# Performance work log

Hardware: AMD Instinct MI355X
Metric: run time of the kernel (lower is better)

Reference implementation:

```python
import jax, jax.numpy as jnp
import numpy as np

NEG_SLOPE = 0.2  # PyG GATConv default


def add_self_loops(edge_index, num_nodes):
    loops = jnp.arange(num_nodes, dtype=edge_index.dtype)
    return jnp.concatenate([edge_index, jnp.stack([loops, loops])], axis=1)


def gat_conv(x, edge_index, W, att_src, att_dst, bias, heads, out_ch, concat):
    # x: [N, F_in]; edge_index: [2, E] with row0=src(j), row1=dst(i)
    N = x.shape[0]
    xl = (x @ W).reshape(N, heads, out_ch)              # [N, H, C]
    src, dst = edge_index[0], edge_index[1]
    a_src = jnp.einsum('nhc,hc->nh', xl, att_src)        # [N, H]
    a_dst = jnp.einsum('nhc,hc->nh', xl, att_dst)        # [N, H]
    alpha = jax.nn.leaky_relu(a_src[src] + a_dst[dst], NEG_SLOPE)  # [E, H]
    # segment softmax over incoming edges of each dst node
    m = jax.ops.segment_max(alpha, dst, num_segments=N)  # [N, H]
    e = jnp.exp(alpha - m[dst])
    denom = jax.ops.segment_sum(e, dst, num_segments=N)
    coef = e / (denom[dst] + 1e-16)                      # [E, H]
    msg = xl[src] * coef[..., None]                      # [E, H, C]
    out = jax.ops.segment_sum(msg, dst, num_segments=N)  # [N, H, C]
    out = out.reshape(N, heads * out_ch) if concat else out.mean(axis=1)
    return out + bias


def setup_inputs() -> dict:
    key = jax.random.key(0)
    ks = jax.random.split(key, 12)
    N, E = 50000, 800000
    nfeat, nhid, nheads, nclass = 512, 8, 8, 16
    hid = nhid * nheads  # 64
    s1 = 1.0 / np.sqrt(nfeat)
    s2 = 1.0 / np.sqrt(hid)
    return {
        'x': jax.random.normal(ks[0], (N, nfeat), jnp.float32),
        'edge_index': jax.random.randint(ks[1], (2, E), 0, N, jnp.int64 if jax.config.jax_enable_x64 else jnp.int32),
        'W1': jax.random.uniform(ks[2], (nfeat, hid), jnp.float32, -s1, s1),
        'att_src1': jax.random.uniform(ks[3], (nheads, nhid), jnp.float32, -s2, s2),
        'att_dst1': jax.random.uniform(ks[4], (nheads, nhid), jnp.float32, -s2, s2),
        'bias1': jnp.zeros((hid,), jnp.float32),
        'W2': jax.random.uniform(ks[5], (hid, nclass), jnp.float32, -s2, s2),
        'att_src2': jax.random.uniform(ks[6], (1, nclass), jnp.float32, -0.25, 0.25),
        'att_dst2': jax.random.uniform(ks[7], (1, nclass), jnp.float32, -0.25, 0.25),
        'bias2': jnp.zeros((nclass,), jnp.float32),
    }


def reference(x, edge_index, W1, att_src1, att_dst1, bias1, W2, att_src2, att_dst2, bias2):
    N = x.shape[0]
    ei = add_self_loops(edge_index, N)
    # dropout layers are identity at inference
    h = gat_conv(x, ei, W1, att_src1, att_dst1, bias1, heads=8, out_ch=8, concat=True)
    o = gat_conv(h, ei, W2, att_src2, att_dst2, bias2, heads=1, out_ch=16, concat=True)
    o = jax.nn.elu(o)
    return jax.nn.log_softmax(o, axis=1)
```

## Files before the change

### kernel.cpp

```cpp
#include <hip/hip_runtime.h>
#include <math.h>

#define NEG_SLOPE 0.2f

typedef short short8 __attribute__((ext_vector_type(8)));
typedef float floatx4 __attribute__((ext_vector_type(4)));

static __device__ __forceinline__ float bf2f(unsigned short u) {
  return __uint_as_float(((unsigned int)u) << 16);
}
static __device__ __forceinline__ unsigned short f2bf(float f) {
  unsigned int u = __float_as_uint(f);
  u = (u + 0x7fffu + ((u >> 16) & 1u)) >> 16;
  return (unsigned short)u;
}
static __device__ __forceinline__ unsigned int pack2(float a, float b) {
  return (unsigned int)f2bf(a) | ((unsigned int)f2bf(b) << 16);
}

__global__ void conv_w1(const float* __restrict__ W1, unsigned short* __restrict__ W1t) {
  int i = blockIdx.x * 256 + threadIdx.x;
  int k = i >> 6, c = i & 63;
  W1t[c * 512 + k] = f2bf(W1[i]);
}

__global__ __launch_bounds__(256) void gemm1_mfma(const float* __restrict__ A,
                                                  const unsigned short* __restrict__ W1t,
                                                  const float* __restrict__ att_src,
                                                  const float* __restrict__ att_dst,
                                                  unsigned short* __restrict__ xlb,
                                                  float* __restrict__ a_src,
                                                  float* __restrict__ a_dst, int M) {
  __shared__ unsigned short As[64 * 72];
  __shared__ unsigned short Bs[64 * 72];
  int tid = threadIdx.x;
  int w = tid >> 6, lane = tid & 63;
  int q = lane >> 4, cl = lane & 15;
  int row0 = blockIdx.x << 6;
  floatx4 acc[4] = {};

  int sr = tid >> 2;
  int skq = (tid & 3) << 4;
  int arow = row0 + sr;
  const float* Aptr = A + (size_t)arow * 512 + skq;
  const unsigned short* Bptr = W1t + sr * 512 + skq;
  unsigned short* AsW = As + sr * 72 + skq;
  unsigned short* BsW = Bs + sr * 72 + skq;

  for (int k0 = 0; k0 < 512; k0 += 64) {
    float4 f0 = make_float4(0.f, 0.f, 0.f, 0.f), f1 = f0, f2 = f0, f3 = f0;
    if (arow < M) {
      f0 = *(const float4*)(Aptr + k0);
      f1 = *(const float4*)(Aptr + k0 + 4);
      f2 = *(const float4*)(Aptr + k0 + 8);
      f3 = *(const float4*)(Aptr + k0 + 12);
    }
    uint4 b0 = *(const uint4*)(Bptr + k0);
    uint4 b1 = *(const uint4*)(Bptr + k0 + 8);
    __syncthreads();
    uint4 a0, a1;
    a0.x = pack2(f0.x, f0.y); a0.y = pack2(f0.z, f0.w);
    a0.z = pack2(f1.x, f1.y); a0.w = pack2(f1.z, f1.w);
    a1.x = pack2(f2.x, f2.y); a1.y = pack2(f2.z, f2.w);
    a1.z = pack2(f3.x, f3.y); a1.w = pack2(f3.z, f3.w);
    *(uint4*)(AsW) = a0;
    *(uint4*)(AsW + 8) = a1;
    *(uint4*)(BsW) = b0;
    *(uint4*)(BsW + 8) = b1;
    __syncthreads();
#pragma unroll
    for (int kk = 0; kk < 2; ++kk) {
      short8 af = *(const short8*)(As + (w * 16 + cl) * 72 + kk * 32 + q * 8);
#pragma unroll
      for (int t = 0; t < 4; ++t) {
        short8 bf = *(const short8*)(Bs + (t * 16 + cl) * 72 + kk * 32 + q * 8);
        acc[t] = __builtin_amdgcn_mfma_f32_16x16x32_bf16(af, bf, acc[t], 0, 0, 0);
      }
    }
  }

  float asv[4], adv[4];
#pragma unroll
  for (int t = 0; t < 4; ++t) {
    asv[t] = att_src[t * 16 + cl];
    adv[t] = att_dst[t * 16 + cl];
  }
#pragma unroll
  for (int reg = 0; reg < 4; ++reg) {
    int r = row0 + w * 16 + q * 4 + reg;
    bool ok = r < M;
#pragma unroll
    for (int t = 0; t < 4; ++t) {
      float v = acc[t][reg];
      if (ok) xlb[(size_t)r * 64 + t * 16 + cl] = f2bf(v);
      float ps = v * asv[t];
      float pd = v * adv[t];
      ps += __shfl_xor(ps, 1); pd += __shfl_xor(pd, 1);
      ps += __shfl_xor(ps, 2); pd += __shfl_xor(pd, 2);
      ps += __shfl_xor(ps, 4); pd += __shfl_xor(pd, 4);
      if (ok && (cl & 7) == 0) {
        int h = t * 2 + (cl >> 3);
        a_src[r * 8 + h] = ps;
        a_dst[r * 8 + h] = pd;
      }
    }
  }
}

__global__ void deg_init(int* __restrict__ deg, int N) {
  int n = blockIdx.x * blockDim.x + threadIdx.x;
  if (n < N) deg[n] = 1;
}

__global__ __launch_bounds__(256) void deg_hist_sliced(const int* __restrict__ ei,
                                                       int* __restrict__ deg,
                                                       int E, int N, int ipc) {
  int slice = blockIdx.x & 7;
  int chunk = blockIdx.x >> 3;
  int lo = (int)(((long long)slice * N) >> 3);
  int hi = (int)(((long long)(slice + 1) * N) >> 3);
  int beg = chunk * ipc;
  int end = min(beg + ipc, E);
  for (int i = beg + threadIdx.x; i < end; i += 256) {
    int d = ei[E + i];
    if (d >= lo && d < hi) atomicAdd(&deg[d], 1);
  }
}

__global__ __launch_bounds__(256) void partial_sums(const int* __restrict__ deg,
                                                    int* __restrict__ partials, int N) {
  __shared__ int ws[4];
  int base = blockIdx.x * 512;
  int tid = threadIdx.x;
  int i0 = base + tid * 2;
  int s = 0;
  if (i0 < N) s += deg[i0];
  if (i0 + 1 < N) s += deg[i0 + 1];
#pragma unroll
  for (int off = 32; off >= 1; off >>= 1) s += __shfl_xor(s, off, 64);
  if ((tid & 63) == 0) ws[tid >> 6] = s;
  __syncthreads();
  if (tid == 0) partials[blockIdx.x] = ws[0] + ws[1] + ws[2] + ws[3];
}

__global__ __launch_bounds__(256) void scan_partials(const int* __restrict__ partials,
                                                     int* __restrict__ blockoff,
                                                     int* __restrict__ rowptr, int nb, int N) {
  __shared__ int sums[256];
  int tid = threadIdx.x;
  int chunk = (nb + 255) >> 8;
  int start = tid * chunk, end = min(start + chunk, nb);
  int s = 0;
  for (int i = start; i < end; ++i) s += partials[i];
  sums[tid] = s;
  __syncthreads();
  for (int off = 1; off < 256; off <<= 1) {
    int t = (tid >= off) ? sums[tid - off] : 0;
    __syncthreads();
    sums[tid] += t;
    __syncthreads();
  }
  int run = (tid == 0) ? 0 : sums[tid - 1];
  for (int i = start; i < end; ++i) {
    blockoff[i] = run;
    run += partials[i];
  }
  if (tid == 255) rowptr[N] = sums[255];
}

__global__ __launch_bounds__(256) void scan_blocks(const int* __restrict__ deg,
                                                   const int* __restrict__ blockoff,
                                                   int* __restrict__ rowptr,
                                                   int* __restrict__ cursor, int N) {
  __shared__ int wavesum[4];
  int base = blockIdx.x * 512;
  int tid = threadIdx.x;
  int lane = tid & 63, wv = tid >> 6;
  int i0 = base + tid * 2;
  int d0 = (i0 < N) ? deg[i0] : 0;
  int d1 = (i0 + 1 < N) ? deg[i0 + 1] : 0;
  int s = d0 + d1;
  int v = s;
#pragma unroll
  for (int off = 1; off < 64; off <<= 1) {
    int t = __shfl_up(v, off, 64);
    if (lane >= off) v += t;
  }
  if (lane == 63) wavesum[wv] = v;
  __syncthreads();
  int woff = 0;
  for (int w = 0; w < wv; ++w) woff += wavesum[w];
  int excl = v - s + woff + blockoff[blockIdx.x];
  if (i0 < N) { rowptr[i0] = excl; cursor[i0] = excl; }
  if (i0 + 1 < N) { rowptr[i0 + 1] = excl + d0; cursor[i0 + 1] = excl + d0; }
}

__global__ __launch_bounds__(256) void scatter_sliced(const int* __restrict__ ei,
                                                      int* __restrict__ cursor,
                                                      int* __restrict__ srcs,
                                                      int E, int N, int ipc) {
  int slice = blockIdx.x & 7;
  int chunk = blockIdx.x >> 3;
  int lo = (int)(((long long)slice * N) >> 3);
  int hi = (int)(((long long)(slice + 1) * N) >> 3);
  int total = E + N;
  int beg = chunk * ipc;
  int end = min(beg + ipc, total);
  for (int i = beg + threadIdx.x; i < end; i += 256) {
    int d = (i < E) ? ei[E + i] : (i - E);
    if (d >= lo && d < hi) {
      int s = (i < E) ? ei[i] : d;
      int pos = atomicAdd(&cursor[d], 1);
      srcs[pos] = s;
    }
  }
}

__global__ __launch_bounds__(256) void agg1_csr(const int* __restrict__ rowptr,
                                                const int* __restrict__ srcs,
                                                const float* __restrict__ a_src,
                                                const float* __restrict__ a_dst,
                                                const unsigned short* __restrict__ xlb,
                                                float* __restrict__ agg1, int N) {
  int wave = (blockIdx.x * blockDim.x + threadIdx.x) >> 6;
  int lane = threadIdx.x & 63;
  if (wave >= N) return;
  int h = lane >> 3;
  int beg = rowptr[wave], end = rowptr[wave + 1];
  float ad = a_dst[wave * 8 + h];
  float den = 0.f, acc = 0.f;
  int p = beg;
  for (; p + 4 <= end; p += 4) {
    int s0 = srcs[p], s1 = srcs[p + 1], s2 = srcs[p + 2], s3 = srcs[p + 3];
    float a0 = a_src[s0 * 8 + h], a1 = a_src[s1 * 8 + h];
    float a2 = a_src[s2 * 8 + h], a3 = a_src[s3 * 8 + h];
    float x0 = bf2f(xlb[(size_t)s0 * 64 + lane]);
    float x1 = bf2f(xlb[(size_t)s1 * 64 + lane]);
    float x2 = bf2f(xlb[(size_t)s2 * 64 + lane]);
    float x3 = bf2f(xlb[(size_t)s3 * 64 + lane]);
    a0 += ad; a1 += ad; a2 += ad; a3 += ad;
    a0 = a0 >= 0.f ? a0 : NEG_SLOPE * a0;
    a1 = a1 >= 0.f ? a1 : NEG_SLOPE * a1;
    a2 = a2 >= 0.f ? a2 : NEG_SLOPE * a2;
    a3 = a3 >= 0.f ? a3 : NEG_SLOPE * a3;
    float w0 = __expf(a0), w1 = __expf(a1), w2 = __expf(a2), w3 = __expf(a3);
    den += (w0 + w1) + (w2 + w3);
    acc += w0 * x0 + w1 * x1 + w2 * x2 + w3 * x3;
  }
  for (; p < end; ++p) {
    int s = srcs[p];
    float a = a_src[s * 8 + h] + ad;
    a = a >= 0.f ? a : NEG_SLOPE * a;
    float w = __expf(a);
    den += w;
    acc += w * bf2f(xlb[(size_t)s * 64 + lane]);
  }
  agg1[(size_t)wave * 64 + lane] = acc / (den + 1e-16f);
}

__global__ __launch_bounds__(256) void gemm2_prep(const float* __restrict__ agg1,
                                                  const float* __restrict__ bias1,
                                                  const float* __restrict__ W2,
                                                  const float* __restrict__ att_src2,
                                                  const float* __restrict__ att_dst2,
                                                  float* __restrict__ xl2,
                                                  float* __restrict__ a_src2,
                                                  float* __restrict__ a_dst2, int N) {
  __shared__ float hs[16 * 68];
  int tid = threadIdx.x;
  int n0 = blockIdx.x << 4;
  {
    int node = tid >> 4;
    int off = (tid & 15) << 2;
    int nn = n0 + node;
    float4 v = make_float4(0.f, 0.f, 0.f, 0.f);
    if (nn < N) {
      v = *(const float4*)(agg1 + (size_t)nn * 64 + off);
      float4 b = *(const float4*)(bias1 + off);
      v.x += b.x; v.y += b.y; v.z += b.z; v.w += b.w;
    }
    *(float4*)(hs + node * 68 + off) = v;
  }
  __syncthreads();
  int t = tid >> 4, c = tid & 15;
  int n = n0 + t;
  if (n >= N) return;
  float sum = 0.f;
#pragma unroll
  for (int k = 0; k < 64; ++k) sum += hs[t * 68 + k] * W2[k * 16 + c];
  xl2[(size_t)n * 16 + c] = sum;
  float ps = sum * att_src2[c];
  float pd = sum * att_dst2[c];
#pragma unroll
  for (int w = 8; w >= 1; w >>= 1) {
    ps += __shfl_xor(ps, w, 16);
    pd += __shfl_xor(pd, w, 16);
  }
  if (c == 0) {
    a_src2[n] = ps;
    a_dst2[n] = pd;
  }
}

__global__ __launch_bounds__(256) void agg2_fin(const int* __restrict__ rowptr,
                                                const int* __restrict__ srcs,
                                                const float* __restrict__ a_src2,
                                                const float* __restrict__ a_dst2,
                                                const float* __restrict__ xl2,
                                                const float* __restrict__ bias2,
                                                float* __restrict__ out, int N) {
  int t = blockIdx.x * blockDim.x + threadIdx.x;
  int node = t >> 4;
  int c = t & 15;
  if (node >= N) return;
  int beg = rowptr[node], end = rowptr[node + 1];
  float ad = a_dst2[node];
  float den = 0.f, acc = 0.f;
  int p = beg;
  for (; p + 4 <= end; p += 4) {
    int s0 = srcs[p], s1 = srcs[p + 1], s2 = srcs[p + 2], s3 = srcs[p + 3];
    float a0 = a_src2[s0], a1 = a_src2[s1], a2 = a_src2[s2], a3 = a_src2[s3];
    float x0 = xl2[(size_t)s0 * 16 + c], x1 = xl2[(size_t)s1 * 16 + c];
    float x2 = xl2[(size_t)s2 * 16 + c], x3 = xl2[(size_t)s3 * 16 + c];
    a0 += ad; a1 += ad; a2 += ad; a3 += ad;
    a0 = a0 >= 0.f ? a0 : NEG_SLOPE * a0;
    a1 = a1 >= 0.f ? a1 : NEG_SLOPE * a1;
    a2 = a2 >= 0.f ? a2 : NEG_SLOPE * a2;
    a3 = a3 >= 0.f ? a3 : NEG_SLOPE * a3;
    float w0 = __expf(a0), w1 = __expf(a1), w2 = __expf(a2), w3 = __expf(a3);
    den += (w0 + w1) + (w2 + w3);
    acc += w0 * x0 + w1 * x1 + w2 * x2 + w3 * x3;
  }
  for (; p < end; ++p) {
    int s = srcs[p];
    float a = a_src2[s] + ad;
    a = a >= 0.f ? a : NEG_SLOPE * a;
    float w = __expf(a);
    den += w;
    acc += w * xl2[(size_t)s * 16 + c];
  }
  float o = acc / (den + 1e-16f) + bias2[c];
  o = o > 0.f ? o : expm1f(o);
  float mx = o;
#pragma unroll
  for (int w = 8; w >= 1; w >>= 1) mx = fmaxf(mx, __shfl_xor(mx, w, 16));
  float e = __expf(o - mx);
  float ssum = e;
#pragma unroll
  for (int w = 8; w >= 1; w >>= 1) ssum += __shfl_xor(ssum, w, 16);
  out[(size_t)node * 16 + c] = o - mx - logf(ssum);
}

extern "C" void kernel_launch(void* const* d_in, const int* in_sizes, int n_in,
                              void* d_out, int out_size, void* d_ws, size_t ws_size,
                              hipStream_t stream) {
  const float* x        = (const float*)d_in[0];
  const int*   ei       = (const int*)d_in[1];
  const float* W1       = (const float*)d_in[2];
  const float* att_src1 = (const float*)d_in[3];
  const float* att_dst1 = (const float*)d_in[4];
  const float* bias1    = (const float*)d_in[5];
  const float* W2       = (const float*)d_in[6];
  const float* att_src2 = (const float*)d_in[7];
  const float* att_dst2 = (const float*)d_in[8];
  const float* bias2    = (const float*)d_in[9];
  float* out = (float*)d_out;

  int N = in_sizes[0] / 512;
  int E = in_sizes[1] / 2;
  int nb = (N + 511) / 512;

  char* ws = (char*)d_ws;
  unsigned short* xlb = (unsigned short*)ws;        ws += (size_t)N * 64 * 2;
  unsigned short* W1t = (unsigned short*)ws;        ws += (size_t)512 * 64 * 2;
  float* a_src1 = (float*)ws;                       ws += (size_t)N * 8 * 4;
  float* a_dst1 = (float*)ws;                       ws += (size_t)N * 8 * 4;
  float* agg1   = (float*)ws;                       ws += (size_t)N * 64 * 4;
  float* xl2    = (float*)ws;                       ws += (size_t)N * 16 * 4;
  float* a_src2 = (float*)ws;                       ws += (size_t)N * 4;
  float* a_dst2 = (float*)ws;                       ws += (size_t)N * 4;
  int* deg      = (int*)ws;                         ws += (size_t)N * 4;
  int* rowptr   = (int*)ws;                         ws += (size_t)(N + 1) * 4;
  int* cursor   = (int*)ws;                         ws += (size_t)N * 4;
  int* srcs     = (int*)ws;                         ws += (size_t)(E + N) * 4;
  int* partials = (int*)ws;                         ws += (size_t)nb * 4;
  int* blockoff = (int*)ws;                         ws += (size_t)nb * 4;

  const int NCHUNK = 256;
  int ipc_h = (E + NCHUNK - 1) / NCHUNK;
  int ipc_s = (E + N + NCHUNK - 1) / NCHUNK;
  deg_init<<<(N + 255) / 256, 256, 0, stream>>>(deg, N);
  deg_hist_sliced<<<NCHUNK * 8, 256, 0, stream>>>(ei, deg, E, N, ipc_h);
  partial_sums<<<nb, 256, 0, stream>>>(deg, partials, N);
  scan_partials<<<1, 256, 0, stream>>>(partials, blockoff, rowptr, nb, N);
  scan_blocks<<<nb, 256, 0, stream>>>(deg, blockoff, rowptr, cursor, N);
  scatter_sliced<<<NCHUNK * 8, 256, 0, stream>>>(ei, cursor, srcs, E, N, ipc_s);

  conv_w1<<<128, 256, 0, stream>>>(W1, W1t);
  gemm1_mfma<<<(N + 63) / 64, 256, 0, stream>>>(x, W1t, att_src1, att_dst1,
                                                xlb, a_src1, a_dst1, N);
  agg1_csr<<<((size_t)N * 64 + 255) / 256, 256, 0, stream>>>(rowptr, srcs, a_src1, a_dst1,
                                                             xlb, agg1, N);

  gemm2_prep<<<(N + 15) / 16, 256, 0, stream>>>(agg1, bias1, W2, att_src2, att_dst2,
                                                xl2, a_src2, a_dst2, N);
  agg2_fin<<<((size_t)N * 16 + 255) / 256, 256, 0, stream>>>(rowptr, srcs, a_src2, a_dst2,
                                                             xl2, bias2, out, N);
}
```

Before: 329.6 us.

## Fuse layer-1 aggregation with layer-2 GEMM, double-buffer gemm1, merge prep kernels

The layer-1 CSR aggregation and the layer-2 projection now run in one kernel, so the N×64 fp32 agg1 intermediate is no longer written and re-read. The W1 conversion and degree initialisation are merged into one launch. gemm1 now double-buffers its LDS tiles so global loads overlap the MFMA work. Both aggregation loops are unrolled from 4 to 8 edges. The cost is more LDS in gemm1 and a fused kernel where only one wave per block does the small GEMM after a barrier.

```diff
diff --git a/kernel.cpp b/kernel.cpp
--- a/kernel.cpp
+++ b/kernel.cpp
@@ -18,10 +18,15 @@
   return (unsigned int)f2bf(a) | ((unsigned int)f2bf(b) << 16);
 }
 
-__global__ void conv_w1(const float* __restrict__ W1, unsigned short* __restrict__ W1t) {
+__global__ void prep_kernel(const float* __restrict__ W1, unsigned short* __restrict__ W1t,
+                            int* __restrict__ deg, int N) {
   int i = blockIdx.x * 256 + threadIdx.x;
-  int k = i >> 6, c = i & 63;
-  W1t[c * 512 + k] = f2bf(W1[i]);
+  if (i < 32768) {
+    int k = i >> 6, c = i & 63;
+    W1t[c * 512 + k] = f2bf(W1[i]);
+  }
+  int j = i - 32768;
+  if (j >= 0 && j < N) deg[j] = 1;
 }
 
 __global__ __launch_bounds__(256) void gemm1_mfma(const float* __restrict__ A,
@@ -31,8 +36,8 @@
                                                   unsigned short* __restrict__ xlb,
                                                   float* __restrict__ a_src,
                                                   float* __restrict__ a_dst, int M) {
-  __shared__ unsigned short As[64 * 72];
-  __shared__ unsigned short Bs[64 * 72];
+  __shared__ unsigned short As[2][64 * 72];
+  __shared__ unsigned short Bs[2][64 * 72];
   int tid = threadIdx.x;
   int w = tid >> 6, lane = tid & 63;
   int q = lane >> 4, cl = lane & 15;
@@ -44,38 +49,69 @@
   int arow = row0 + sr;
   const float* Aptr = A + (size_t)arow * 512 + skq;
   const unsigned short* Bptr = W1t + sr * 512 + skq;
-  unsigned short* AsW = As + sr * 72 + skq;
-  unsigned short* BsW = Bs + sr * 72 + skq;
-
-  for (int k0 = 0; k0 < 512; k0 += 64) {
-    float4 f0 = make_float4(0.f, 0.f, 0.f, 0.f), f1 = f0, f2 = f0, f3 = f0;
-    if (arow < M) {
-      f0 = *(const float4*)(Aptr + k0);
-      f1 = *(const float4*)(Aptr + k0 + 4);
-      f2 = *(const float4*)(Aptr + k0 + 8);
-      f3 = *(const float4*)(Aptr + k0 + 12);
-    }
-    uint4 b0 = *(const uint4*)(Bptr + k0);
-    uint4 b1 = *(const uint4*)(Bptr + k0 + 8);
-    __syncthreads();
+  unsigned short* AsW0 = &As[0][sr * 72 + skq];
+  unsigned short* BsW0 = &Bs[0][sr * 72 + skq];
+  unsigned short* AsW1 = &As[1][sr * 72 + skq];
+  unsigned short* BsW1 = &Bs[1][sr * 72 + skq];
+
+  float4 f0 = make_float4(0.f, 0.f, 0.f, 0.f), f1 = f0, f2 = f0, f3 = f0;
+  uint4 b0, b1;
+  if (arow < M) {
+    f0 = *(const float4*)(Aptr);
+    f1 = *(const float4*)(Aptr + 4);
+    f2 = *(const float4*)(Aptr + 8);
+    f3 = *(const float4*)(Aptr + 12);
+  }
+  b0 = *(const uint4*)(Bptr);
+  b1 = *(const uint4*)(Bptr + 8);
+  {
     uint4 a0, a1;
     a0.x = pack2(f0.x, f0.y); a0.y = pack2(f0.z, f0.w);
     a0.z = pack2(f1.x, f1.y); a0.w = pack2(f1.z, f1.w);
     a1.x = pack2(f2.x, f2.y); a1.y = pack2(f2.z, f2.w);
     a1.z = pack2(f3.x, f3.y); a1.w = pack2(f3.z, f3.w);
-    *(uint4*)(AsW) = a0;
-    *(uint4*)(AsW + 8) = a1;
-    *(uint4*)(BsW) = b0;
-    *(uint4*)(BsW + 8) = b1;
-    __syncthreads();
+    *(uint4*)(AsW0) = a0;
+    *(uint4*)(AsW0 + 8) = a1;
+    *(uint4*)(BsW0) = b0;
+    *(uint4*)(BsW0 + 8) = b1;
+  }
+  __syncthreads();
+
+  for (int c = 0; c < 8; ++c) {
+    int cur = c & 1;
+    if (c < 7) {
+      int k0 = (c + 1) << 6;
+      if (arow < M) {
+        f0 = *(const float4*)(Aptr + k0);
+        f1 = *(const float4*)(Aptr + k0 + 4);
+        f2 = *(const float4*)(Aptr + k0 + 8);
+        f3 = *(const float4*)(Aptr + k0 + 12);
+      }
+      b0 = *(const uint4*)(Bptr + k0);
+      b1 = *(const uint4*)(Bptr + k0 + 8);
+    }
 #pragma unroll
     for (int kk = 0; kk < 2; ++kk) {
-      short8 af = *(const short8*)(As + (w * 16 + cl) * 72 + kk * 32 + q * 8);
+      short8 af = *(const short8*)(&As[cur][(w * 16 + cl) * 72 + kk * 32 + q * 8]);
 #pragma unroll
       for (int t = 0; t < 4; ++t) {
-        short8 bf = *(const short8*)(Bs + (t * 16 + cl) * 72 + kk * 32 + q * 8);
+        short8 bf = *(const short8*)(&Bs[cur][(t * 16 + cl) * 72 + kk * 32 + q * 8]);
         acc[t] = __builtin_amdgcn_mfma_f32_16x16x32_bf16(af, bf, acc[t], 0, 0, 0);
       }
+    }
+    if (c < 7) {
+      uint4 a0, a1;
+      a0.x = pack2(f0.x, f0.y); a0.y = pack2(f0.z, f0.w);
+      a0.z = pack2(f1.x, f1.y); a0.w = pack2(f1.z, f1.w);
+      a1.x = pack2(f2.x, f2.y); a1.y = pack2(f2.z, f2.w);
+      a1.z = pack2(f3.x, f3.y); a1.w = pack2(f3.z, f3.w);
+      unsigned short* AsW = cur ? AsW0 : AsW1;
+      unsigned short* BsW = cur ? BsW0 : BsW1;
+      *(uint4*)(AsW) = a0;
+      *(uint4*)(AsW + 8) = a1;
+      *(uint4*)(BsW) = b0;
+      *(uint4*)(BsW + 8) = b1;
+      __syncthreads();
     }
   }
 
@@ -105,11 +141,6 @@
       }
     }
   }
-}
-
-__global__ void deg_init(int* __restrict__ deg, int N) {
-  int n = blockIdx.x * blockDim.x + threadIdx.x;
-  if (n < N) deg[n] = 1;
 }
 
 __global__ __launch_bounds__(256) void deg_hist_sliced(const int* __restrict__ ei,
@@ -216,49 +247,11 @@
   }
 }
 
-__global__ __launch_bounds__(256) void agg1_csr(const int* __restrict__ rowptr,
-                                                const int* __restrict__ srcs,
-                                                const float* __restrict__ a_src,
-                                                const float* __restrict__ a_dst,
-                                                const unsigned short* __restrict__ xlb,
-                                                float* __restrict__ agg1, int N) {
-  int wave = (blockIdx.x * blockDim.x + threadIdx.x) >> 6;
-  int lane = threadIdx.x & 63;
-  if (wave >= N) return;
-  int h = lane >> 3;
-  int beg = rowptr[wave], end = rowptr[wave + 1];
-  float ad = a_dst[wave * 8 + h];
-  float den = 0.f, acc = 0.f;
-  int p = beg;
-  for (; p + 4 <= end; p += 4) {
-    int s0 = srcs[p], s1 = srcs[p + 1], s2 = srcs[p + 2], s3 = srcs[p + 3];
-    float a0 = a_src[s0 * 8 + h], a1 = a_src[s1 * 8 + h];
-    float a2 = a_src[s2 * 8 + h], a3 = a_src[s3 * 8 + h];
-    float x0 = bf2f(xlb[(size_t)s0 * 64 + lane]);
-    float x1 = bf2f(xlb[(size_t)s1 * 64 + lane]);
-    float x2 = bf2f(xlb[(size_t)s2 * 64 + lane]);
-    float x3 = bf2f(xlb[(size_t)s3 * 64 + lane]);
-    a0 += ad; a1 += ad; a2 += ad; a3 += ad;
-    a0 = a0 >= 0.f ? a0 : NEG_SLOPE * a0;
-    a1 = a1 >= 0.f ? a1 : NEG_SLOPE * a1;
-    a2 = a2 >= 0.f ? a2 : NEG_SLOPE * a2;
-    a3 = a3 >= 0.f ? a3 : NEG_SLOPE * a3;
-    float w0 = __expf(a0), w1 = __expf(a1), w2 = __expf(a2), w3 = __expf(a3);
-    den += (w0 + w1) + (w2 + w3);
-    acc += w0 * x0 + w1 * x1 + w2 * x2 + w3 * x3;
-  }
-  for (; p < end; ++p) {
-    int s = srcs[p];
-    float a = a_src[s * 8 + h] + ad;
-    a = a >= 0.f ? a : NEG_SLOPE * a;
-    float w = __expf(a);
-    den += w;
-    acc += w * bf2f(xlb[(size_t)s * 64 + lane]);
-  }
-  agg1[(size_t)wave * 64 + lane] = acc / (den + 1e-16f);
-}
-
-__global__ __launch_bounds__(256) void gemm2_prep(const float* __restrict__ agg1,
+__global__ __launch_bounds__(256) void agg1_fused(const int* __restrict__ rowptr,
+                                                  const int* __restrict__ srcs,
+                                                  const float* __restrict__ a_src,
+                                                  const float* __restrict__ a_dst,
+                                                  const unsigned short* __restrict__ xlb,
                                                   const float* __restrict__ bias1,
                                                   const float* __restrict__ W2,
                                                   const float* __restrict__ att_src2,
@@ -266,39 +259,81 @@
                                                   float* __restrict__ xl2,
                                                   float* __restrict__ a_src2,
                                                   float* __restrict__ a_dst2, int N) {
-  __shared__ float hs[16 * 68];
+  __shared__ float W2s[64 * 16];
+  __shared__ float hs[4][72];
   int tid = threadIdx.x;
-  int n0 = blockIdx.x << 4;
-  {
-    int node = tid >> 4;
-    int off = (tid & 15) << 2;
-    int nn = n0 + node;
-    float4 v = make_float4(0.f, 0.f, 0.f, 0.f);
-    if (nn < N) {
-      v = *(const float4*)(agg1 + (size_t)nn * 64 + off);
-      float4 b = *(const float4*)(bias1 + off);
-      v.x += b.x; v.y += b.y; v.z += b.z; v.w += b.w;
-    }
-    *(float4*)(hs + node * 68 + off) = v;
+  for (int i = tid; i < 1024; i += 256) W2s[i] = W2[i];
+  int wv = tid >> 6, lane = tid & 63;
+  int node0 = blockIdx.x << 2;
+  int node = node0 + wv;
+  if (node < N) {
+    int h = lane >> 3;
+    int beg = rowptr[node], end = rowptr[node + 1];
+    float ad = a_dst[node * 8 + h];
+    float den = 0.f, acc = 0.f;
+    int p = beg;
+    for (; p + 8 <= end; p += 8) {
+      int s0 = srcs[p], s1 = srcs[p + 1], s2 = srcs[p + 2], s3 = srcs[p + 3];
+      int s4 = srcs[p + 4], s5 = srcs[p + 5], s6 = srcs[p + 6], s7 = srcs[p + 7];
+      float a0 = a_src[s0 * 8 + h], a1 = a_src[s1 * 8 + h];
+      float a2 = a_src[s2 * 8 + h], a3 = a_src[s3 * 8 + h];
+      float a4 = a_src[s4 * 8 + h], a5 = a_src[s5 * 8 + h];
+      float a6 = a_src[s6 * 8 + h], a7 = a_src[s7 * 8 + h];
+      float x0 = bf2f(xlb[(size_t)s0 * 64 + lane]);
+      float x1 = bf2f(xlb[(size_t)s1 * 64 + lane]);
+      float x2 = bf2f(xlb[(size_t)s2 * 64 + lane]);
+      float x3 = bf2f(xlb[(size_t)s3 * 64 + lane]);
+      float x4 = bf2f(xlb[(size_t)s4 * 64 + lane]);
+      float x5 = bf2f(xlb[(size_t)s5 * 64 + lane]);
+      float x6 = bf2f(xlb[(size_t)s6 * 64 + lane]);
+      float x7 = bf2f(xlb[(size_t)s7 * 64 + lane]);
+      a0 += ad; a1 += ad; a2 += ad; a3 += ad;
+      a4 += ad; a5 += ad; a6 += ad; a7 += ad;
+      a0 = a0 >= 0.f ? a0 : NEG_SLOPE * a0;
+      a1 = a1 >= 0.f ? a1 : NEG_SLOPE * a1;
+      a2 = a2 >= 0.f ? a2 : NEG_SLOPE * a2;
+      a3 = a3 >= 0.f ? a3 : NEG_SLOPE * a3;
+      a4 = a4 >= 0.f ? a4 : NEG_SLOPE * a4;
+      a5 = a5 >= 0.f ? a5 : NEG_SLOPE * a5;
+      a6 = a6 >= 0.f ? a6 : NEG_SLOPE * a6;
+      a7 = a7 >= 0.f ? a7 : NEG_SLOPE * a7;
+      float w0 = __expf(a0), w1 = __expf(a1), w2 = __expf(a2), w3 = __expf(a3);
+      float w4 = __expf(a4), w5 = __expf(a5), w6 = __expf(a6), w7 = __expf(a7);
+      den += ((w0 + w1) + (w2 + w3)) + ((w4 + w5) + (w6 + w7));
+      acc += w0 * x0 + w1 * x1 + w2 * x2 + w3 * x3;
+      acc += w4 * x4 + w5 * x5 + w6 * x6 + w7 * x7;
+    }
+    for (; p < end; ++p) {
+      int s = srcs[p];
+      float a = a_src[s * 8 + h] + ad;
+      a = a >= 0.f ? a : NEG_SLOPE * a;
+      float w = __expf(a);
+      den += w;
+      acc += w * bf2f(xlb[(size_t)s * 64 + lane]);
+    }
+    hs[wv][lane] = acc / (den + 1e-16f) + bias1[lane];
   }
   __syncthreads();
-  int t = tid >> 4, c = tid & 15;
-  int n = n0 + t;
-  if (n >= N) return;
-  float sum = 0.f;
-#pragma unroll
-  for (int k = 0; k < 64; ++k) sum += hs[t * 68 + k] * W2[k * 16 + c];
-  xl2[(size_t)n * 16 + c] = sum;
-  float ps = sum * att_src2[c];
-  float pd = sum * att_dst2[c];
-#pragma unroll
-  for (int w = 8; w >= 1; w >>= 1) {
-    ps += __shfl_xor(ps, w, 16);
-    pd += __shfl_xor(pd, w, 16);
-  }
-  if (c == 0) {
-    a_src2[n] = ps;
-    a_dst2[n] = pd;
+  if (tid < 64) {
+    int nd = tid >> 4, c = tid & 15;
+    int n = node0 + nd;
+    if (n < N) {
+      float sum = 0.f;
+#pragma unroll
+      for (int k = 0; k < 64; ++k) sum += hs[nd][k] * W2s[k * 16 + c];
+      xl2[(size_t)n * 16 + c] = sum;
+      float ps = sum * att_src2[c];
+      float pd = sum * att_dst2[c];
+#pragma unroll
+      for (int w = 8; w >= 1; w >>= 1) {
+        ps += __shfl_xor(ps, w, 16);
+        pd += __shfl_xor(pd, w, 16);
+      }
+      if (c == 0) {
+        a_src2[n] = ps;
+        a_dst2[n] = pd;
+      }
+    }
   }
 }
 
@@ -317,19 +352,30 @@
   float ad = a_dst2[node];
   float den = 0.f, acc = 0.f;
   int p = beg;
-  for (; p + 4 <= end; p += 4) {
+  for (; p + 8 <= end; p += 8) {
     int s0 = srcs[p], s1 = srcs[p + 1], s2 = srcs[p + 2], s3 = srcs[p + 3];
+    int s4 = srcs[p + 4], s5 = srcs[p + 5], s6 = srcs[p + 6], s7 = srcs[p + 7];
     float a0 = a_src2[s0], a1 = a_src2[s1], a2 = a_src2[s2], a3 = a_src2[s3];
+    float a4 = a_src2[s4], a5 = a_src2[s5], a6 = a_src2[s6], a7 = a_src2[s7];
     float x0 = xl2[(size_t)s0 * 16 + c], x1 = xl2[(size_t)s1 * 16 + c];
     float x2 = xl2[(size_t)s2 * 16 + c], x3 = xl2[(size_t)s3 * 16 + c];
+    float x4 = xl2[(size_t)s4 * 16 + c], x5 = xl2[(size_t)s5 * 16 + c];
+    float x6 = xl2[(size_t)s6 * 16 + c], x7 = xl2[(size_t)s7 * 16 + c];
     a0 += ad; a1 += ad; a2 += ad; a3 += ad;
+    a4 += ad; a5 += ad; a6 += ad; a7 += ad;
     a0 = a0 >= 0.f ? a0 : NEG_SLOPE * a0;
     a1 = a1 >= 0.f ? a1 : NEG_SLOPE * a1;
     a2 = a2 >= 0.f ? a2 : NEG_SLOPE * a2;
     a3 = a3 >= 0.f ? a3 : NEG_SLOPE * a3;
+    a4 = a4 >= 0.f ? a4 : NEG_SLOPE * a4;
+    a5 = a5 >= 0.f ? a5 : NEG_SLOPE * a5;
+    a6 = a6 >= 0.f ? a6 : NEG_SLOPE * a6;
+    a7 = a7 >= 0.f ? a7 : NEG_SLOPE * a7;
     float w0 = __expf(a0), w1 = __expf(a1), w2 = __expf(a2), w3 = __expf(a3);
-    den += (w0 + w1) + (w2 + w3);
+    float w4 = __expf(a4), w5 = __expf(a5), w6 = __expf(a6), w7 = __expf(a7);
+    den += ((w0 + w1) + (w2 + w3)) + ((w4 + w5) + (w6 + w7));
     acc += w0 * x0 + w1 * x1 + w2 * x2 + w3 * x3;
+    acc += w4 * x4 + w5 * x5 + w6 * x6 + w7 * x7;
   }
   for (; p < end; ++p) {
     int s = srcs[p];
@@ -375,7 +421,6 @@
   unsigned short* W1t = (unsigned short*)ws;        ws += (size_t)512 * 64 * 2;
   float* a_src1 = (float*)ws;                       ws += (size_t)N * 8 * 4;
   float* a_dst1 = (float*)ws;                       ws += (size_t)N * 8 * 4;
-  float* agg1   = (float*)ws;                       ws += (size_t)N * 64 * 4;
   float* xl2    = (float*)ws;                       ws += (size_t)N * 16 * 4;
   float* a_src2 = (float*)ws;                       ws += (size_t)N * 4;
   float* a_dst2 = (float*)ws;                       ws += (size_t)N * 4;
@@ -389,21 +434,19 @@
   const int NCHUNK = 256;
   int ipc_h = (E + NCHUNK - 1) / NCHUNK;
   int ipc_s = (E + N + NCHUNK - 1) / NCHUNK;
-  deg_init<<<(N + 255) / 256, 256, 0, stream>>>(deg, N);
+
+  prep_kernel<<<(32768 + N + 255) / 256, 256, 0, stream>>>(W1, W1t, deg, N);
   deg_hist_sliced<<<NCHUNK * 8, 256, 0, stream>>>(ei, deg, E, N, ipc_h);
   partial_sums<<<nb, 256, 0, stream>>>(deg, partials, N);
   scan_partials<<<1, 256, 0, stream>>>(partials, blockoff, rowptr, nb, N);
   scan_blocks<<<nb, 256, 0, stream>>>(deg, blockoff, rowptr, cursor, N);
   scatter_sliced<<<NCHUNK * 8, 256, 0, stream>>>(ei, cursor, srcs, E, N, ipc_s);
 
-  conv_w1<<<128, 256, 0, stream>>>(W1, W1t);
   gemm1_mfma<<<(N + 63) / 64, 256, 0, stream>>>(x, W1t, att_src1, att_dst1,
                                                 xlb, a_src1, a_dst1, N);
-  agg1_csr<<<((size_t)N * 64 + 255) / 256, 256, 0, stream>>>(rowptr, srcs, a_src1, a_dst1,
-                                                             xlb, agg1, N);
-
-  gemm2_prep<<<(N + 15) / 16, 256, 0, stream>>>(agg1, bias1, W2, att_src2, att_dst2,
-                                                xl2, a_src2, a_dst2, N);
+  agg1_fused<<<(N + 3) / 4, 256, 0, stream>>>(rowptr, srcs, a_src1, a_dst1, xlb,
+                                              bias1, W2, att_src2, att_dst2,
+                                              xl2, a_src2, a_dst2, N);
   agg2_fin<<<((size_t)N * 16 + 255) / 256, 256, 0, stream>>>(rowptr, srcs, a_src2, a_dst2,
                                                              xl2, bias2, out, N);
 }
```

New measurement: 330.7 us. No clear change (+0.3%).

## Fuse layer-2 GEMM into aggregation, use 16-bit indices, merge prep kernels

Applied to the files above, without the earlier changes.

Fuses gemm2_prep into the layer-1 aggregation kernel, so each wave computes its node's 16 outputs with cross-lane shuffles and the agg1 buffer is no longer written or read. Edge indices are narrowed to 16-bit (src16/dst16/srcs), which is only valid because N=50000 fits in 16 bits. The W1 conversion, degree init and index narrowing are merged into one prep kernel. The layer-1 gather loop is unrolled to 8 edges, and agg2 switches to one wave per node with four edge groups. The cost is a 96-step shuffle reduction per node and an index format that breaks for N>65535.

```diff
diff --git a/kernel.cpp b/kernel.cpp
--- a/kernel.cpp
+++ b/kernel.cpp
@@ -1,4 +1,5 @@
 #include <hip/hip_runtime.h>
+#include <hip/hip_bf16.h>
 #include <math.h>
 
 #define NEG_SLOPE 0.2f
@@ -15,13 +16,28 @@
   return (unsigned short)u;
 }
 static __device__ __forceinline__ unsigned int pack2(float a, float b) {
-  return (unsigned int)f2bf(a) | ((unsigned int)f2bf(b) << 16);
-}
-
-__global__ void conv_w1(const float* __restrict__ W1, unsigned short* __restrict__ W1t) {
+  __hip_bfloat162 h = __float22bfloat162_rn(make_float2(a, b));
+  unsigned int u;
+  __builtin_memcpy(&u, &h, 4);
+  return u;
+}
+
+__global__ void prep_kernel(const float* __restrict__ W1, unsigned short* __restrict__ W1t,
+                            int* __restrict__ deg, const int* __restrict__ ei,
+                            unsigned short* __restrict__ src16, unsigned short* __restrict__ dst16,
+                            int N, int E) {
   int i = blockIdx.x * 256 + threadIdx.x;
-  int k = i >> 6, c = i & 63;
-  W1t[c * 512 + k] = f2bf(W1[i]);
+  if (i < 32768) {
+    int k = i >> 6, c = i & 63;
+    W1t[c * 512 + k] = f2bf(W1[i]);
+  }
+  int j = i - 32768;
+  if (j >= 0 && j < N) deg[j] = 1;
+  int e = i - 32768 - N;
+  if (e >= 0 && e < E) {
+    src16[e] = (unsigned short)ei[e];
+    dst16[e] = (unsigned short)ei[E + e];
+  }
 }
 
 __global__ __launch_bounds__(256) void gemm1_mfma(const float* __restrict__ A,
@@ -107,12 +123,7 @@
   }
 }
 
-__global__ void deg_init(int* __restrict__ deg, int N) {
-  int n = blockIdx.x * blockDim.x + threadIdx.x;
-  if (n < N) deg[n] = 1;
-}
-
-__global__ __launch_bounds__(256) void deg_hist_sliced(const int* __restrict__ ei,
+__global__ __launch_bounds__(256) void deg_hist_sliced(const unsigned short* __restrict__ dst16,
                                                        int* __restrict__ deg,
                                                        int E, int N, int ipc) {
   int slice = blockIdx.x & 7;
@@ -122,7 +133,7 @@
   int beg = chunk * ipc;
   int end = min(beg + ipc, E);
   for (int i = beg + threadIdx.x; i < end; i += 256) {
-    int d = ei[E + i];
+    int d = dst16[i];
     if (d >= lo && d < hi) atomicAdd(&deg[d], 1);
   }
 }
@@ -195,9 +206,10 @@
   if (i0 + 1 < N) { rowptr[i0 + 1] = excl + d0; cursor[i0 + 1] = excl + d0; }
 }
 
-__global__ __launch_bounds__(256) void scatter_sliced(const int* __restrict__ ei,
+__global__ __launch_bounds__(256) void scatter_sliced(const unsigned short* __restrict__ src16,
+                                                      const unsigned short* __restrict__ dst16,
                                                       int* __restrict__ cursor,
-                                                      int* __restrict__ srcs,
+                                                      unsigned short* __restrict__ srcs,
                                                       int E, int N, int ipc) {
   int slice = blockIdx.x & 7;
   int chunk = blockIdx.x >> 3;
@@ -207,21 +219,27 @@
   int beg = chunk * ipc;
   int end = min(beg + ipc, total);
   for (int i = beg + threadIdx.x; i < end; i += 256) {
-    int d = (i < E) ? ei[E + i] : (i - E);
+    int d = (i < E) ? (int)dst16[i] : (i - E);
     if (d >= lo && d < hi) {
-      int s = (i < E) ? ei[i] : d;
+      int s = (i < E) ? (int)src16[i] : d;
       int pos = atomicAdd(&cursor[d], 1);
-      srcs[pos] = s;
+      srcs[pos] = (unsigned short)s;
     }
   }
 }
 
-__global__ __launch_bounds__(256) void agg1_csr(const int* __restrict__ rowptr,
-                                                const int* __restrict__ srcs,
-                                                const float* __restrict__ a_src,
-                                                const float* __restrict__ a_dst,
-                                                const unsigned short* __restrict__ xlb,
-                                                float* __restrict__ agg1, int N) {
+__global__ __launch_bounds__(256) void agg1_wave(const int* __restrict__ rowptr,
+                                                 const unsigned short* __restrict__ srcs,
+                                                 const float* __restrict__ a_src,
+                                                 const float* __restrict__ a_dst,
+                                                 const unsigned short* __restrict__ xlb,
+                                                 const float* __restrict__ bias1,
+                                                 const float* __restrict__ W2,
+                                                 const float* __restrict__ att_src2,
+                                                 const float* __restrict__ att_dst2,
+                                                 float* __restrict__ xl2,
+                                                 float* __restrict__ a_src2,
+                                                 float* __restrict__ a_dst2, int N) {
   int wave = (blockIdx.x * blockDim.x + threadIdx.x) >> 6;
   int lane = threadIdx.x & 63;
   if (wave >= N) return;
@@ -230,22 +248,36 @@
   float ad = a_dst[wave * 8 + h];
   float den = 0.f, acc = 0.f;
   int p = beg;
-  for (; p + 4 <= end; p += 4) {
+  for (; p + 8 <= end; p += 8) {
     int s0 = srcs[p], s1 = srcs[p + 1], s2 = srcs[p + 2], s3 = srcs[p + 3];
+    int s4 = srcs[p + 4], s5 = srcs[p + 5], s6 = srcs[p + 6], s7 = srcs[p + 7];
     float a0 = a_src[s0 * 8 + h], a1 = a_src[s1 * 8 + h];
     float a2 = a_src[s2 * 8 + h], a3 = a_src[s3 * 8 + h];
+    float a4 = a_src[s4 * 8 + h], a5 = a_src[s5 * 8 + h];
+    float a6 = a_src[s6 * 8 + h], a7 = a_src[s7 * 8 + h];
     float x0 = bf2f(xlb[(size_t)s0 * 64 + lane]);
     float x1 = bf2f(xlb[(size_t)s1 * 64 + lane]);
     float x2 = bf2f(xlb[(size_t)s2 * 64 + lane]);
     float x3 = bf2f(xlb[(size_t)s3 * 64 + lane]);
+    float x4 = bf2f(xlb[(size_t)s4 * 64 + lane]);
+    float x5 = bf2f(xlb[(size_t)s5 * 64 + lane]);
+    float x6 = bf2f(xlb[(size_t)s6 * 64 + lane]);
+    float x7 = bf2f(xlb[(size_t)s7 * 64 + lane]);
     a0 += ad; a1 += ad; a2 += ad; a3 += ad;
+    a4 += ad; a5 += ad; a6 += ad; a7 += ad;
     a0 = a0 >= 0.f ? a0 : NEG_SLOPE * a0;
     a1 = a1 >= 0.f ? a1 : NEG_SLOPE * a1;
     a2 = a2 >= 0.f ? a2 : NEG_SLOPE * a2;
     a3 = a3 >= 0.f ? a3 : NEG_SLOPE * a3;
+    a4 = a4 >= 0.f ? a4 : NEG_SLOPE * a4;
+    a5 = a5 >= 0.f ? a5 : NEG_SLOPE * a5;
+    a6 = a6 >= 0.f ? a6 : NEG_SLOPE * a6;
+    a7 = a7 >= 0.f ? a7 : NEG_SLOPE * a7;
     float w0 = __expf(a0), w1 = __expf(a1), w2 = __expf(a2), w3 = __expf(a3);
-    den += (w0 + w1) + (w2 + w3);
+    float w4 = __expf(a4), w5 = __expf(a5), w6 = __expf(a6), w7 = __expf(a7);
+    den += ((w0 + w1) + (w2 + w3)) + ((w4 + w5) + (w6 + w7));
     acc += w0 * x0 + w1 * x1 + w2 * x2 + w3 * x3;
+    acc += w4 * x4 + w5 * x5 + w6 * x6 + w7 * x7;
   }
   for (; p < end; ++p) {
     int s = srcs[p];
@@ -255,90 +287,70 @@
     den += w;
     acc += w * bf2f(xlb[(size_t)s * 64 + lane]);
   }
-  agg1[(size_t)wave * 64 + lane] = acc / (den + 1e-16f);
-}
-
-__global__ __launch_bounds__(256) void gemm2_prep(const float* __restrict__ agg1,
-                                                  const float* __restrict__ bias1,
-                                                  const float* __restrict__ W2,
-                                                  const float* __restrict__ att_src2,
-                                                  const float* __restrict__ att_dst2,
-                                                  float* __restrict__ xl2,
-                                                  float* __restrict__ a_src2,
-                                                  float* __restrict__ a_dst2, int N) {
-  __shared__ float hs[16 * 68];
-  int tid = threadIdx.x;
-  int n0 = blockIdx.x << 4;
-  {
-    int node = tid >> 4;
-    int off = (tid & 15) << 2;
-    int nn = n0 + node;
-    float4 v = make_float4(0.f, 0.f, 0.f, 0.f);
-    if (nn < N) {
-      v = *(const float4*)(agg1 + (size_t)nn * 64 + off);
-      float4 b = *(const float4*)(bias1 + off);
-      v.x += b.x; v.y += b.y; v.z += b.z; v.w += b.w;
-    }
-    *(float4*)(hs + node * 68 + off) = v;
-  }
-  __syncthreads();
-  int t = tid >> 4, c = tid & 15;
-  int n = n0 + t;
-  if (n >= N) return;
-  float sum = 0.f;
-#pragma unroll
-  for (int k = 0; k < 64; ++k) sum += hs[t * 68 + k] * W2[k * 16 + c];
-  xl2[(size_t)n * 16 + c] = sum;
-  float ps = sum * att_src2[c];
-  float pd = sum * att_dst2[c];
+  float hv = acc / (den + 1e-16f) + bias1[lane];
+
+  const float4* w2p = (const float4*)(W2 + lane * 16);
+  float4 wa = w2p[0], wb = w2p[1], wc = w2p[2], wd = w2p[3];
+  float t[16];
+  t[0] = hv * wa.x; t[1] = hv * wa.y; t[2] = hv * wa.z; t[3] = hv * wa.w;
+  t[4] = hv * wb.x; t[5] = hv * wb.y; t[6] = hv * wb.z; t[7] = hv * wb.w;
+  t[8] = hv * wc.x; t[9] = hv * wc.y; t[10] = hv * wc.z; t[11] = hv * wc.w;
+  t[12] = hv * wd.x; t[13] = hv * wd.y; t[14] = hv * wd.z; t[15] = hv * wd.w;
+#pragma unroll
+  for (int off = 1; off < 64; off <<= 1) {
+#pragma unroll
+    for (int c = 0; c < 16; ++c) t[c] += __shfl_xor(t[c], off);
+  }
+  int cl = lane & 15;
+  float val = t[0];
+#pragma unroll
+  for (int c = 1; c < 16; ++c) val = (cl == c) ? t[c] : val;
+  float ps = val * att_src2[cl];
+  float pd = val * att_dst2[cl];
 #pragma unroll
   for (int w = 8; w >= 1; w >>= 1) {
     ps += __shfl_xor(ps, w, 16);
     pd += __shfl_xor(pd, w, 16);
   }
-  if (c == 0) {
-    a_src2[n] = ps;
-    a_dst2[n] = pd;
+  if (lane < 16) xl2[(size_t)wave * 16 + lane] = val;
+  if (lane == 0) {
+    a_src2[wave] = ps;
+    a_dst2[wave] = pd;
   }
 }
 
 __global__ __launch_bounds__(256) void agg2_fin(const int* __restrict__ rowptr,
-                                                const int* __restrict__ srcs,
+                                                const unsigned short* __restrict__ srcs,
                                                 const float* __restrict__ a_src2,
                                                 const float* __restrict__ a_dst2,
                                                 const float* __restrict__ xl2,
                                                 const float* __restrict__ bias2,
                                                 float* __restrict__ out, int N) {
-  int t = blockIdx.x * blockDim.x + threadIdx.x;
-  int node = t >> 4;
-  int c = t & 15;
-  if (node >= N) return;
-  int beg = rowptr[node], end = rowptr[node + 1];
-  float ad = a_dst2[node];
+  int wave = (blockIdx.x * blockDim.x + threadIdx.x) >> 6;
+  int lane = threadIdx.x & 63;
+  if (wave >= N) return;
+  int j = lane >> 4, c = lane & 15;
+  int beg = rowptr[wave], end = rowptr[wave + 1];
+  float ad = a_dst2[wave];
   float den = 0.f, acc = 0.f;
-  int p = beg;
-  for (; p + 4 <= end; p += 4) {
-    int s0 = srcs[p], s1 = srcs[p + 1], s2 = srcs[p + 2], s3 = srcs[p + 3];
-    float a0 = a_src2[s0], a1 = a_src2[s1], a2 = a_src2[s2], a3 = a_src2[s3];
-    float x0 = xl2[(size_t)s0 * 16 + c], x1 = xl2[(size_t)s1 * 16 + c];
-    float x2 = xl2[(size_t)s2 * 16 + c], x3 = xl2[(size_t)s3 * 16 + c];
-    a0 += ad; a1 += ad; a2 += ad; a3 += ad;
+  for (int p0 = beg; p0 < end; p0 += 8) {
+    int pe0 = p0 + j, pe1 = p0 + 4 + j;
+    bool v0 = pe0 < end, v1 = pe1 < end;
+    int s0 = v0 ? (int)srcs[pe0] : 0;
+    int s1 = v1 ? (int)srcs[pe1] : 0;
+    float a0 = a_src2[s0] + ad;
+    float a1 = a_src2[s1] + ad;
+    float x0 = xl2[(size_t)s0 * 16 + c];
+    float x1 = xl2[(size_t)s1 * 16 + c];
     a0 = a0 >= 0.f ? a0 : NEG_SLOPE * a0;
     a1 = a1 >= 0.f ? a1 : NEG_SLOPE * a1;
-    a2 = a2 >= 0.f ? a2 : NEG_SLOPE * a2;
-    a3 = a3 >= 0.f ? a3 : NEG_SLOPE * a3;
-    float w0 = __expf(a0), w1 = __expf(a1), w2 = __expf(a2), w3 = __expf(a3);
-    den += (w0 + w1) + (w2 + w3);
-    acc += w0 * x0 + w1 * x1 + w2 * x2 + w3 * x3;
-  }
-  for (; p < end; ++p) {
-    int s = srcs[p];
-    float a = a_src2[s] + ad;
-    a = a >= 0.f ? a : NEG_SLOPE * a;
-    float w = __expf(a);
-    den += w;
-    acc += w * xl2[(size_t)s * 16 + c];
-  }
+    float w0 = v0 ? __expf(a0) : 0.f;
+    float w1 = v1 ? __expf(a1) : 0.f;
+    den += w0 + w1;
+    acc += w0 * x0 + w1 * x1;
+  }
+  den += __shfl_xor(den, 16); den += __shfl_xor(den, 32);
+  acc += __shfl_xor(acc, 16); acc += __shfl_xor(acc, 32);
   float o = acc / (den + 1e-16f) + bias2[c];
   o = o > 0.f ? o : expm1f(o);
   float mx = o;
@@ -348,7 +360,7 @@
   float ssum = e;
 #pragma unroll
   for (int w = 8; w >= 1; w >>= 1) ssum += __shfl_xor(ssum, w, 16);
-  out[(size_t)node * 16 + c] = o - mx - logf(ssum);
+  if (lane < 16) out[(size_t)wave * 16 + c] = o - mx - logf(ssum);
 }
 
 extern "C" void kernel_launch(void* const* d_in, const int* in_sizes, int n_in,
@@ -370,40 +382,44 @@
   int E = in_sizes[1] / 2;
   int nb = (N + 511) / 512;
 
-  char* ws = (char*)d_ws;
-  unsigned short* xlb = (unsigned short*)ws;        ws += (size_t)N * 64 * 2;
-  unsigned short* W1t = (unsigned short*)ws;        ws += (size_t)512 * 64 * 2;
-  float* a_src1 = (float*)ws;                       ws += (size_t)N * 8 * 4;
-  float* a_dst1 = (float*)ws;                       ws += (size_t)N * 8 * 4;
-  float* agg1   = (float*)ws;                       ws += (size_t)N * 64 * 4;
-  float* xl2    = (float*)ws;                       ws += (size_t)N * 16 * 4;
-  float* a_src2 = (float*)ws;                       ws += (size_t)N * 4;
-  float* a_dst2 = (float*)ws;                       ws += (size_t)N * 4;
-  int* deg      = (int*)ws;                         ws += (size_t)N * 4;
-  int* rowptr   = (int*)ws;                         ws += (size_t)(N + 1) * 4;
-  int* cursor   = (int*)ws;                         ws += (size_t)N * 4;
-  int* srcs     = (int*)ws;                         ws += (size_t)(E + N) * 4;
-  int* partials = (int*)ws;                         ws += (size_t)nb * 4;
-  int* blockoff = (int*)ws;                         ws += (size_t)nb * 4;
+  char* wsp = (char*)d_ws;
+  auto alloc = [&](size_t bytes) {
+    char* p = wsp;
+    wsp += (bytes + 255) & ~(size_t)255;
+    return p;
+  };
+  unsigned short* xlb   = (unsigned short*)alloc((size_t)N * 64 * 2);
+  unsigned short* W1t   = (unsigned short*)alloc((size_t)512 * 64 * 2);
+  float* a_src1 = (float*)alloc((size_t)N * 8 * 4);
+  float* a_dst1 = (float*)alloc((size_t)N * 8 * 4);
+  float* xl2    = (float*)alloc((size_t)N * 16 * 4);
+  float* a_src2 = (float*)alloc((size_t)N * 4);
+  float* a_dst2 = (float*)alloc((size_t)N * 4);
+  int* deg      = (int*)alloc((size_t)N * 4);
+  int* rowptr   = (int*)alloc((size_t)(N + 1) * 4);
+  int* cursor   = (int*)alloc((size_t)N * 4);
+  int* partials = (int*)alloc((size_t)nb * 4);
+  int* blockoff = (int*)alloc((size_t)nb * 4);
+  unsigned short* src16 = (unsigned short*)alloc((size_t)E * 2);
+  unsigned short* dst16 = (unsigned short*)alloc((size_t)E * 2);
+  unsigned short* srcs  = (unsigned short*)alloc((size_t)(E + N) * 2);
 
   const int NCHUNK = 256;
   int ipc_h = (E + NCHUNK - 1) / NCHUNK;
   int ipc_s = (E + N + NCHUNK - 1) / NCHUNK;
-  deg_init<<<(N + 255) / 256, 256, 0, stream>>>(deg, N);
-  deg_hist_sliced<<<NCHUNK * 8, 256, 0, stream>>>(ei, deg, E, N, ipc_h);
+
+  prep_kernel<<<(32768 + N + E + 255) / 256, 256, 0, stream>>>(W1, W1t, deg, ei, src16, dst16, N, E);
+  deg_hist_sliced<<<NCHUNK * 8, 256, 0, stream>>>(dst16, deg, E, N, ipc_h);
   partial_sums<<<nb, 256, 0, stream>>>(deg, partials, N);
   scan_partials<<<1, 256, 0, stream>>>(partials, blockoff, rowptr, nb, N);
   scan_blocks<<<nb, 256, 0, stream>>>(deg, blockoff, rowptr, cursor, N);
-  scatter_sliced<<<NCHUNK * 8, 256, 0, stream>>>(ei, cursor, srcs, E, N, ipc_s);
-
-  conv_w1<<<128, 256, 0, stream>>>(W1, W1t);
+  scatter_sliced<<<NCHUNK * 8, 256, 0, stream>>>(src16, dst16, cursor, srcs, E, N, ipc_s);
+
   gemm1_mfma<<<(N + 63) / 64, 256, 0, stream>>>(x, W1t, att_src1, att_dst1,
                                                 xlb, a_src1, a_dst1, N);
-  agg1_csr<<<((size_t)N * 64 + 255) / 256, 256, 0, stream>>>(rowptr, srcs, a_src1, a_dst1,
-                                                             xlb, agg1, N);
-
-  gemm2_prep<<<(N + 15) / 16, 256, 0, stream>>>(agg1, bias1, W2, att_src2, att_dst2,
-                                                xl2, a_src2, a_dst2, N);
-  agg2_fin<<<((size_t)N * 16 + 255) / 256, 256, 0, stream>>>(rowptr, srcs, a_src2, a_dst2,
+  agg1_wave<<<((size_t)N * 64 + 255) / 256, 256, 0, stream>>>(rowptr, srcs, a_src1, a_dst1, xlb,
+                                                              bias1, W2, att_src2, att_dst2,
+                                                              xl2, a_src2, a_dst2, N);
+  agg2_fin<<<((size_t)N * 64 + 255) / 256, 256, 0, stream>>>(rowptr, srcs, a_src2, a_dst2,
                                                              xl2, bias2, out, N);
 }
```

Measured after the change: 351.2 us. +6.5%, slower.
